# Performance work log

Measured on AMD Instinct MI355X. Metric: run time of the kernel, lower is better.

Reference implementation:

```python
import jax, jax.numpy as jnp
import numpy as np

LATENT_DIM = 256
CODEBOOK_SIZE = 8192


def setup_inputs() -> dict:
    key = jax.random.key(0)
    k1, k2 = jax.random.split(key)
    z_e = jax.random.normal(k1, (16, 32, 32, LATENT_DIM), dtype=jnp.float32)
    codebook = jax.random.normal(k2, (CODEBOOK_SIZE, LATENT_DIM), dtype=jnp.float32)
    return {"z_e": z_e, "codebook": codebook}


def reference(z_e, codebook):
    orig_shape = z_e.shape
    z_flat = z_e.reshape(-1, LATENT_DIM)                      # [N, D]
    # squared distances via ||z||^2 + ||e||^2 - 2 z.e^T  -> [N, K]
    dists = (jnp.sum(z_flat ** 2, axis=1, keepdims=True)
             + jnp.sum(codebook ** 2, axis=1)
             - 2.0 * jnp.matmul(z_flat, codebook.T))
    idx = jnp.argmin(dists, axis=1)                           # [N]
    z_q = codebook[idx].reshape(orig_shape)                   # gather + reshape
    commitment_loss = jnp.mean((jax.lax.stop_gradient(z_q) - z_e) ** 2)
    codebook_loss = jnp.mean((z_q - jax.lax.stop_gradient(z_e)) ** 2)
    loss = commitment_loss + codebook_loss
    z_q_st = z_e + jax.lax.stop_gradient(z_q - z_e)           # straight-through
    return (z_e, loss, z_q_st)
```

## Files before the change

kernel.cpp:

```cpp
#include <hip/hip_runtime.h>
#include <stdint.h>

typedef short short8 __attribute__((ext_vector_type(8)));
typedef float f32x4 __attribute__((ext_vector_type(4)));

#define DDIM 256
#define NROWS 16384
#define KCB 8192
#define KSPLIT 4
#define KC 2048
#define ND 4194304

__device__ __forceinline__ void gll16(const void* g, void* l) {
    __builtin_amdgcn_global_load_lds(
        (const __attribute__((address_space(1))) unsigned int*)g,
        (__attribute__((address_space(3))) unsigned int*)l, 16, 0, 0);
}

__device__ __forceinline__ unsigned short bf16_rne(float x) {
    unsigned u = __float_as_uint(x);
    unsigned r = (u + 0x7FFFu + ((u >> 16) & 1u)) >> 16;
    return (unsigned short)r;
}

__global__ void k_prep(const float* __restrict__ z, const float* __restrict__ cb,
                       unsigned short* __restrict__ zh, unsigned short* __restrict__ zl,
                       unsigned short* __restrict__ eh, unsigned short* __restrict__ el,
                       float* __restrict__ norms) {
    const int b = blockIdx.x, t = threadIdx.x;
    const bool isz = (b < 4096);
    const float* src = isz ? z : cb;
    unsigned short* hi = isz ? zh : eh;
    unsigned short* lo = isz ? zl : el;
    const int i = (isz ? b : (b - 4096)) * 256 + t;
    float4 v = reinterpret_cast<const float4*>(src)[i];
    ushort4 h, l;
    h.x = bf16_rne(v.x); l.x = bf16_rne(v.x - __uint_as_float((unsigned)h.x << 16));
    h.y = bf16_rne(v.y); l.y = bf16_rne(v.y - __uint_as_float((unsigned)h.y << 16));
    h.z = bf16_rne(v.z); l.z = bf16_rne(v.z - __uint_as_float((unsigned)h.z << 16));
    h.w = bf16_rne(v.w); l.w = bf16_rne(v.w - __uint_as_float((unsigned)h.w << 16));
    reinterpret_cast<ushort4*>(hi)[i] = h;
    reinterpret_cast<ushort4*>(lo)[i] = l;
    if (!isz) {
        float s = v.x * v.x + v.y * v.y + v.z * v.z + v.w * v.w;
#pragma unroll
        for (int off = 32; off > 0; off >>= 1) s += __shfl_xor(s, off, 64);
        if ((t & 63) == 0) norms[i >> 6] = s;
    }
}

__device__ __forceinline__ void stageB(char* sdst, const char* pe, const char* pl, int voff0) {
    gll16(pe + voff0,         sdst);
    gll16(pe + voff0 + 16384, sdst + 4096);
    gll16(pl + voff0,         sdst + 8192);
    gll16(pl + voff0 + 16384, sdst + 12288);
}

__launch_bounds__(256, 2)
__global__ void k_score(const unsigned short* __restrict__ zh, const unsigned short* __restrict__ zl,
                        const unsigned short* __restrict__ eh, const unsigned short* __restrict__ el,
                        const float* __restrict__ norms,
                        float* __restrict__ cand_val, int* __restrict__ cand_idx) {
    __shared__ char smem[32768];

    const int rb = blockIdx.x;
    const int ks = blockIdx.y;
    const int t = threadIdx.x, w = t >> 6, lane = t & 63;
    const int l15 = lane & 15, l4 = lane >> 4;

    const int colq = t >> 3;
    const int voff0 = colq * 512 + (((t & 7) ^ (colq & 7)) * 16);

    int voffB[2];
#pragma unroll
    for (int kc = 0; kc < 2; ++kc)
        voffB[kc] = l15 * 128 + ((((kc * 4) + l4) ^ (lane & 7)) * 16);

    short8 Ah[2][8], Al[2][8];
    {
        const size_t base0 = ((size_t)(rb * 128 + w * 32 + l15)) * DDIM + l4 * 8;
#pragma unroll
        for (int r = 0; r < 2; ++r)
#pragma unroll
            for (int kk = 0; kk < 8; ++kk) {
                Ah[r][kk] = *reinterpret_cast<const short8*>(zh + base0 + r * 16 * DDIM + kk * 32);
                Al[r][kk] = *reinterpret_cast<const short8*>(zl + base0 + r * 16 * DDIM + kk * 32);
            }
    }

    float v1[8], v2[8]; unsigned pk[8];
#pragma unroll
    for (int s = 0; s < 8; ++s) { v1[s] = 3.4e38f; v2[s] = 3.4e38f; pk[s] = 0; }

    size_t ub = (size_t)(ks * KC) * 512;
    stageB(smem + t * 16, (const char*)eh + ub, (const char*)el + ub, voff0);
    __syncthreads();

    for (int ct = 0; ct < 32; ++ct) {
        f32x4 acc[2][4];
#pragma unroll
        for (int r = 0; r < 2; ++r)
#pragma unroll
            for (int cf = 0; cf < 4; ++cf) acc[r][cf] = (f32x4){0.f, 0.f, 0.f, 0.f};

#pragma unroll
        for (int dc = 0; dc < 4; ++dc) {
            const int p = dc & 1;
            if (dc < 3) {
                stageB(smem + (p ^ 1) * 16384 + t * 16,
                       (const char*)eh + ub + (dc + 1) * 128,
                       (const char*)el + ub + (dc + 1) * 128, voff0);
            } else if (ct < 31) {
                stageB(smem + (p ^ 1) * 16384 + t * 16,
                       (const char*)eh + ub + 32768,
                       (const char*)el + ub + 32768, voff0);
            }
            const char* cb0 = smem + p * 16384;
#pragma unroll
            for (int cf = 0; cf < 4; ++cf) {
#pragma unroll
                for (int kc = 0; kc < 2; ++kc) {
                    short8 bh = *reinterpret_cast<const short8*>(cb0 + cf * 2048 + voffB[kc]);
                    short8 bl = *reinterpret_cast<const short8*>(cb0 + 8192 + cf * 2048 + voffB[kc]);
                    const int kk = dc * 2 + kc;
#pragma unroll
                    for (int r = 0; r < 2; ++r) {
                        acc[r][cf] = __builtin_amdgcn_mfma_f32_16x16x32_bf16(Ah[r][kk], bh, acc[r][cf], 0, 0, 0);
                        acc[r][cf] = __builtin_amdgcn_mfma_f32_16x16x32_bf16(Ah[r][kk], bl, acc[r][cf], 0, 0, 0);
                        acc[r][cf] = __builtin_amdgcn_mfma_f32_16x16x32_bf16(Al[r][kk], bh, acc[r][cf], 0, 0, 0);
                    }
                }
            }
            __syncthreads();
        }

        {
            const int nb = ks * KC + ct * 64 + l15;
            const float nn0 = norms[nb], nn1 = norms[nb + 16];
            const float nn2 = norms[nb + 32], nn3 = norms[nb + 48];
            const int cl0 = ct * 64 + l15;
#pragma unroll
            for (int r = 0; r < 2; ++r)
#pragma unroll
                for (int reg = 0; reg < 4; ++reg) {
                    float s0 = fmaf(-2.f, acc[r][0][reg], nn0);
                    float s1 = fmaf(-2.f, acc[r][1][reg], nn1);
                    float s2 = fmaf(-2.f, acc[r][2][reg], nn2);
                    float s3 = fmaf(-2.f, acc[r][3][reg], nn3);
                    float sm = s0; int sj = cl0;
                    if (s1 < sm) { sm = s1; sj = cl0 + 16; }
                    if (s2 < sm) { sm = s2; sj = cl0 + 32; }
                    if (s3 < sm) { sm = s3; sj = cl0 + 48; }
                    const int s = r * 4 + reg;
                    if (sm < v1[s]) { v2[s] = v1[s]; pk[s] = (pk[s] << 16) | (unsigned)sj; v1[s] = sm; }
                    else if (sm < v2[s]) { v2[s] = sm; pk[s] = (pk[s] & 0xFFFFu) | ((unsigned)sj << 16); }
                }
        }
        ub += 32768;
    }

#pragma unroll
    for (int m = 1; m < 16; m <<= 1) {
#pragma unroll
        for (int s = 0; s < 8; ++s) {
            float ov1 = __shfl_xor(v1[s], m, 64);
            float ov2 = __shfl_xor(v2[s], m, 64);
            unsigned opk = (unsigned)__shfl_xor((int)pk[s], m, 64);
            const int ia = (int)(pk[s] & 0xFFFFu), ib = (int)(opk & 0xFFFFu);
            bool bl = (ov1 < v1[s]) || (ov1 == v1[s] && ib < ia);
            float f1 = bl ? ov1 : v1[s]; int fi = bl ? ib : ia;
            float rv = bl ? v1[s] : ov1; int ri = bl ? ia : ib;
            float sv = bl ? ov2 : v2[s]; int si = bl ? (int)(opk >> 16) : (int)(pk[s] >> 16);
            bool b2 = (sv < rv) || (sv == rv && si < ri);
            v1[s] = f1; v2[s] = b2 ? sv : rv;
            pk[s] = (unsigned)fi | ((unsigned)(b2 ? si : ri) << 16);
        }
    }
    if (l15 == 0) {
#pragma unroll
        for (int s = 0; s < 8; ++s) {
            const int row = (s >> 2) * 16 + l4 * 4 + (s & 3);
            const int n = rb * 128 + w * 32 + row;
            cand_val[n * 8 + ks * 2 + 0] = v1[s];
            cand_val[n * 8 + ks * 2 + 1] = v2[s];
            cand_idx[n * 8 + ks * 2 + 0] = ks * KC + (int)(pk[s] & 0xFFFFu);
            cand_idx[n * 8 + ks * 2 + 1] = ks * KC + (int)(pk[s] >> 16);
        }
    }
}

__global__ void k_merge(const float* __restrict__ z, const float* __restrict__ cb,
                        const float* __restrict__ norms,
                        const float* __restrict__ cand_val, const int* __restrict__ cand_idx,
                        int* __restrict__ fidx) {
    const int gid = blockIdx.x * blockDim.x + threadIdx.x;
    const int wid = gid >> 6;
    const int lane = threadIdx.x & 63;
    float v1 = 3.4e38f, v2 = 3.4e38f; int i1 = 0, i2 = 0;
#pragma unroll
    for (int c = 0; c < 8; ++c) {
        float v = cand_val[wid * 8 + c]; int i = cand_idx[wid * 8 + c];
        bool lt1 = (v < v1) || (v == v1 && i < i1);
        bool lt2 = (v < v2) || (v == v2 && i < i2);
        if (lt1) { v2 = v1; i2 = i1; v1 = v; i1 = i; }
        else if (lt2) { v2 = v; i2 = i; }
    }
    const float4 zq = *reinterpret_cast<const float4*>(z + (size_t)wid * DDIM + lane * 4);
    float d[2]; int ii[2] = { i1, i2 };
#pragma unroll
    for (int c = 0; c < 2; ++c) {
        const float4 e4 = *reinterpret_cast<const float4*>(cb + (size_t)ii[c] * DDIM + lane * 4);
        float s = zq.x * e4.x + zq.y * e4.y + zq.z * e4.z + zq.w * e4.w;
#pragma unroll
        for (int m = 32; m > 0; m >>= 1) s += __shfl_xor(s, m, 64);
        d[c] = norms[ii[c]] - 2.f * s;
    }
    const int best = (d[1] < d[0] || (d[1] == d[0] && ii[1] < ii[0])) ? ii[1] : ii[0];
    if (lane == 0) fidx[wid] = best;
}

__global__ void k_finalize(const float* __restrict__ z, const float* __restrict__ cb,
                           const int* __restrict__ fidx, float* __restrict__ out,
                           float* __restrict__ partials) {
    const int i4 = blockIdx.x * blockDim.x + threadIdx.x;
    float4 zv = *reinterpret_cast<const float4*>(z + (size_t)i4 * 4);
    *reinterpret_cast<float4*>(out + (size_t)i4 * 4) = zv;
    const int n = i4 >> 6;
    const int d0 = (i4 & 63) << 2;
    const int idx = fidx[n];
    float4 q = *reinterpret_cast<const float4*>(cb + (size_t)idx * DDIM + d0);
    float* oq = out + (size_t)ND + 1 + (size_t)i4 * 4;
    oq[0] = q.x; oq[1] = q.y; oq[2] = q.z; oq[3] = q.w;
    const float dx = q.x - zv.x, dy = q.y - zv.y, dz = q.z - zv.z, dw = q.w - zv.w;
    float s = dx * dx + dy * dy + dz * dz + dw * dw;
#pragma unroll
    for (int off = 32; off > 0; off >>= 1) s += __shfl_xor(s, off, 64);
    __shared__ float sm[4];
    const int wv = threadIdx.x >> 6, ln = threadIdx.x & 63;
    if (ln == 0) sm[wv] = s;
    __syncthreads();
    if (threadIdx.x == 0) partials[blockIdx.x] = sm[0] + sm[1] + sm[2] + sm[3];
}

__global__ void k_loss(const float* __restrict__ partials, float* __restrict__ out) {
    float s = 0.f;
    for (int i = threadIdx.x; i < 4096; i += 256) s += partials[i];
#pragma unroll
    for (int off = 32; off > 0; off >>= 1) s += __shfl_xor(s, off, 64);
    __shared__ float sm[4];
    const int wv = threadIdx.x >> 6, ln = threadIdx.x & 63;
    if (ln == 0) sm[wv] = s;
    __syncthreads();
    if (threadIdx.x == 0) out[ND] = 2.0f * (sm[0] + sm[1] + sm[2] + sm[3]) / (float)ND;
}

extern "C" void kernel_launch(void* const* d_in, const int* in_sizes, int n_in,
                              void* d_out, int out_size, void* d_ws, size_t ws_size,
                              hipStream_t stream) {
    const float* z = (const float*)d_in[0];
    const float* cb = (const float*)d_in[1];
    float* out = (float*)d_out;
    float* ws = (float*)d_ws;

    float* norms = ws;
    int* fidx = (int*)(ws + 8192);
    float* partials = ws + 8192 + 16384;

    char* ob = (char*)d_out;
    unsigned short* zh = (unsigned short*)(ob);
    unsigned short* zl = (unsigned short*)(ob + 8388608);
    unsigned short* eh = (unsigned short*)(ob + 16777216);
    unsigned short* el = (unsigned short*)(ob + 20971520);
    float* cand_val = (float*)(ob + 25165824);
    int* cand_idx = (int*)(ob + 25690112);

    k_prep<<<dim3(6144), dim3(256), 0, stream>>>(z, cb, zh, zl, eh, el, norms);
    k_score<<<dim3(128, 4), dim3(256), 0, stream>>>(zh, zl, eh, el, norms, cand_val, cand_idx);
    k_merge<<<dim3(4096), dim3(256), 0, stream>>>(z, cb, norms, cand_val, cand_idx, fidx);
    k_finalize<<<dim3(4096), dim3(256), 0, stream>>>(z, cb, fidx, out, partials);
    k_loss<<<dim3(1), dim3(256), 0, stream>>>(partials, out);
}
```

Measured before the change: 272.1 us.

## Deepen codebook LDS pipeline to four stages with explicit waitcnt barriers

Replaces the two-buffer LDS double-buffering in the scoring kernel with a four-slot ring that keeps three chunks of codebook loads in flight. Each chunk ends with a partial vmcnt wait and a raw barrier instead of a full __syncthreads, and the MFMA block runs at raised wave priority. Candidate outputs are staged through LDS so they can be written with a coalesced pattern, and indices are masked in the downstream kernels. LDS doubles to 64KB per block, which may limit how many blocks fit per CU alongside the launch bound of 2.

```diff
diff --git a/kernel.cpp b/kernel.cpp
--- a/kernel.cpp
+++ b/kernel.cpp
@@ -49,19 +49,12 @@
     }
 }
 
-__device__ __forceinline__ void stageB(char* sdst, const char* pe, const char* pl, int voff0) {
-    gll16(pe + voff0,         sdst);
-    gll16(pe + voff0 + 16384, sdst + 4096);
-    gll16(pl + voff0,         sdst + 8192);
-    gll16(pl + voff0 + 16384, sdst + 12288);
-}
-
 __launch_bounds__(256, 2)
 __global__ void k_score(const unsigned short* __restrict__ zh, const unsigned short* __restrict__ zl,
                         const unsigned short* __restrict__ eh, const unsigned short* __restrict__ el,
                         const float* __restrict__ norms,
                         float* __restrict__ cand_val, int* __restrict__ cand_idx) {
-    __shared__ char smem[32768];
+    __shared__ char smem[65536];
 
     const int rb = blockIdx.x;
     const int ks = blockIdx.y;
@@ -88,76 +81,102 @@
             }
     }
 
+    const char* pe = (const char*)eh + (size_t)(ks * KC) * 512;
+    const char* pl = (const char*)el + (size_t)(ks * KC) * 512;
+
+    auto stage = [&](int s) {
+        const int off = (s >> 2) * 32768 + (s & 3) * 128;
+        char* sdst = smem + (s & 3) * 16384 + t * 16;
+        gll16(pe + off + voff0,         sdst);
+        gll16(pe + off + voff0 + 16384, sdst + 4096);
+        gll16(pl + off + voff0,         sdst + 8192);
+        gll16(pl + off + voff0 + 16384, sdst + 12288);
+    };
+
     float v1[8], v2[8]; unsigned pk[8];
 #pragma unroll
     for (int s = 0; s < 8; ++s) { v1[s] = 3.4e38f; v2[s] = 3.4e38f; pk[s] = 0; }
 
-    size_t ub = (size_t)(ks * KC) * 512;
-    stageB(smem + t * 16, (const char*)eh + ub, (const char*)el + ub, voff0);
-    __syncthreads();
-
-    for (int ct = 0; ct < 32; ++ct) {
-        f32x4 acc[2][4];
-#pragma unroll
-        for (int r = 0; r < 2; ++r)
-#pragma unroll
-            for (int cf = 0; cf < 4; ++cf) acc[r][cf] = (f32x4){0.f, 0.f, 0.f, 0.f};
-
-#pragma unroll
-        for (int dc = 0; dc < 4; ++dc) {
-            const int p = dc & 1;
-            if (dc < 3) {
-                stageB(smem + (p ^ 1) * 16384 + t * 16,
-                       (const char*)eh + ub + (dc + 1) * 128,
-                       (const char*)el + ub + (dc + 1) * 128, voff0);
-            } else if (ct < 31) {
-                stageB(smem + (p ^ 1) * 16384 + t * 16,
-                       (const char*)eh + ub + 32768,
-                       (const char*)el + ub + 32768, voff0);
-            }
-            const char* cb0 = smem + p * 16384;
-#pragma unroll
-            for (int cf = 0; cf < 4; ++cf) {
-#pragma unroll
-                for (int kc = 0; kc < 2; ++kc) {
-                    short8 bh = *reinterpret_cast<const short8*>(cb0 + cf * 2048 + voffB[kc]);
-                    short8 bl = *reinterpret_cast<const short8*>(cb0 + 8192 + cf * 2048 + voffB[kc]);
-                    const int kk = dc * 2 + kc;
-#pragma unroll
-                    for (int r = 0; r < 2; ++r) {
-                        acc[r][cf] = __builtin_amdgcn_mfma_f32_16x16x32_bf16(Ah[r][kk], bh, acc[r][cf], 0, 0, 0);
-                        acc[r][cf] = __builtin_amdgcn_mfma_f32_16x16x32_bf16(Ah[r][kk], bl, acc[r][cf], 0, 0, 0);
-                        acc[r][cf] = __builtin_amdgcn_mfma_f32_16x16x32_bf16(Al[r][kk], bh, acc[r][cf], 0, 0, 0);
-                    }
+    f32x4 acc[2][4];
+
+    auto compute = [&](int dc) {
+        const char* cb0 = smem + dc * 16384;
+        __builtin_amdgcn_s_setprio(1);
+#pragma unroll
+        for (int cf = 0; cf < 4; ++cf) {
+#pragma unroll
+            for (int kc = 0; kc < 2; ++kc) {
+                short8 bh = *reinterpret_cast<const short8*>(cb0 + cf * 2048 + voffB[kc]);
+                short8 bl = *reinterpret_cast<const short8*>(cb0 + 8192 + cf * 2048 + voffB[kc]);
+                const int kk = dc * 2 + kc;
+#pragma unroll
+                for (int r = 0; r < 2; ++r) {
+                    acc[r][cf] = __builtin_amdgcn_mfma_f32_16x16x32_bf16(Ah[r][kk], bh, acc[r][cf], 0, 0, 0);
+                    acc[r][cf] = __builtin_amdgcn_mfma_f32_16x16x32_bf16(Ah[r][kk], bl, acc[r][cf], 0, 0, 0);
+                    acc[r][cf] = __builtin_amdgcn_mfma_f32_16x16x32_bf16(Al[r][kk], bh, acc[r][cf], 0, 0, 0);
                 }
             }
-            __syncthreads();
         }
-
-        {
-            const int nb = ks * KC + ct * 64 + l15;
-            const float nn0 = norms[nb], nn1 = norms[nb + 16];
-            const float nn2 = norms[nb + 32], nn3 = norms[nb + 48];
-            const int cl0 = ct * 64 + l15;
-#pragma unroll
-            for (int r = 0; r < 2; ++r)
-#pragma unroll
-                for (int reg = 0; reg < 4; ++reg) {
-                    float s0 = fmaf(-2.f, acc[r][0][reg], nn0);
-                    float s1 = fmaf(-2.f, acc[r][1][reg], nn1);
-                    float s2 = fmaf(-2.f, acc[r][2][reg], nn2);
-                    float s3 = fmaf(-2.f, acc[r][3][reg], nn3);
-                    float sm = s0; int sj = cl0;
-                    if (s1 < sm) { sm = s1; sj = cl0 + 16; }
-                    if (s2 < sm) { sm = s2; sj = cl0 + 32; }
-                    if (s3 < sm) { sm = s3; sj = cl0 + 48; }
-                    const int s = r * 4 + reg;
-                    if (sm < v1[s]) { v2[s] = v1[s]; pk[s] = (pk[s] << 16) | (unsigned)sj; v1[s] = sm; }
-                    else if (sm < v2[s]) { v2[s] = sm; pk[s] = (pk[s] & 0xFFFFu) | ((unsigned)sj << 16); }
-                }
+        __builtin_amdgcn_s_setprio(0);
+    };
+
+    auto fold = [&](int ct) {
+        const int nb = ks * KC + ct * 64 + l15;
+        const float nn0 = norms[nb], nn1 = norms[nb + 16];
+        const float nn2 = norms[nb + 32], nn3 = norms[nb + 48];
+        const int cl0 = ct * 64 + l15;
+#pragma unroll
+        for (int r = 0; r < 2; ++r)
+#pragma unroll
+            for (int reg = 0; reg < 4; ++reg) {
+                float s0 = fmaf(-2.f, acc[r][0][reg], nn0);
+                float s1 = fmaf(-2.f, acc[r][1][reg], nn1);
+                float s2 = fmaf(-2.f, acc[r][2][reg], nn2);
+                float s3 = fmaf(-2.f, acc[r][3][reg], nn3);
+                float sm = s0; int sj = cl0;
+                if (s1 < sm) { sm = s1; sj = cl0 + 16; }
+                if (s2 < sm) { sm = s2; sj = cl0 + 32; }
+                if (s3 < sm) { sm = s3; sj = cl0 + 48; }
+                const int s = r * 4 + reg;
+                if (sm < v1[s]) { v2[s] = v1[s]; pk[s] = (pk[s] << 16) | (unsigned)sj; v1[s] = sm; }
+                else if (sm < v2[s]) { v2[s] = sm; pk[s] = (pk[s] & 0xFFFFu) | ((unsigned)sj << 16); }
+            }
+    };
+
+#define ACC_ZERO() do { \
+    _Pragma("unroll") for (int r = 0; r < 2; ++r) \
+    _Pragma("unroll") for (int cf = 0; cf < 4; ++cf) acc[r][cf] = (f32x4){0.f,0.f,0.f,0.f}; } while (0)
+
+#define SYNC_V8()  do { asm volatile("s_waitcnt vmcnt(8) lgkmcnt(0)" ::: "memory"); \
+    __builtin_amdgcn_sched_barrier(0); __builtin_amdgcn_s_barrier(); } while (0)
+#define SYNC_V4()  do { asm volatile("s_waitcnt vmcnt(4) lgkmcnt(0)" ::: "memory"); \
+    __builtin_amdgcn_sched_barrier(0); __builtin_amdgcn_s_barrier(); } while (0)
+#define SYNC_V0()  do { asm volatile("s_waitcnt vmcnt(0) lgkmcnt(0)" ::: "memory"); \
+    __builtin_amdgcn_sched_barrier(0); __builtin_amdgcn_s_barrier(); } while (0)
+
+    stage(0); stage(1); stage(2);
+    asm volatile("s_waitcnt vmcnt(8)" ::: "memory");
+    __builtin_amdgcn_sched_barrier(0);
+    __builtin_amdgcn_s_barrier();
+
+#pragma unroll 1
+    for (int ct = 0; ct < 31; ++ct) {
+        ACC_ZERO();
+        const int s0 = ct * 4;
+#pragma unroll
+        for (int dc = 0; dc < 4; ++dc) {
+            stage(s0 + dc + 3);
+            compute(dc);
+            SYNC_V8();
         }
-        ub += 32768;
-    }
+        fold(ct);
+    }
+    ACC_ZERO();
+    stage(127); compute(0); SYNC_V8();
+    compute(1);             SYNC_V4();
+    compute(2);             SYNC_V0();
+    compute(3);
+    fold(31);
 
 #pragma unroll
     for (int m = 1; m < 16; m <<= 1) {
@@ -176,16 +195,25 @@
             pk[s] = (unsigned)fi | ((unsigned)(b2 ? si : ri) << 16);
         }
     }
+    __syncthreads();
     if (l15 == 0) {
 #pragma unroll
         for (int s = 0; s < 8; ++s) {
             const int row = (s >> 2) * 16 + l4 * 4 + (s & 3);
-            const int n = rb * 128 + w * 32 + row;
-            cand_val[n * 8 + ks * 2 + 0] = v1[s];
-            cand_val[n * 8 + ks * 2 + 1] = v2[s];
-            cand_idx[n * 8 + ks * 2 + 0] = ks * KC + (int)(pk[s] & 0xFFFFu);
-            cand_idx[n * 8 + ks * 2 + 1] = ks * KC + (int)(pk[s] >> 16);
+            const int n = w * 32 + row;
+            reinterpret_cast<int4*>(smem)[n] =
+                make_int4(__float_as_int(v1[s]), (int)(pk[s] & 0xFFFFu),
+                          __float_as_int(v2[s]), (int)(pk[s] >> 16));
         }
+    }
+    __syncthreads();
+    if (t < 128) {
+        int4 A = reinterpret_cast<int4*>(smem)[t];
+        const int n = rb * 128 + t;
+        cand_val[n * 8 + ks * 2 + 0] = __int_as_float(A.x);
+        cand_val[n * 8 + ks * 2 + 1] = __int_as_float(A.z);
+        cand_idx[n * 8 + ks * 2 + 0] = ks * KC + A.y;
+        cand_idx[n * 8 + ks * 2 + 1] = ks * KC + A.w;
     }
 }
 
@@ -199,7 +227,7 @@
     float v1 = 3.4e38f, v2 = 3.4e38f; int i1 = 0, i2 = 0;
 #pragma unroll
     for (int c = 0; c < 8; ++c) {
-        float v = cand_val[wid * 8 + c]; int i = cand_idx[wid * 8 + c];
+        float v = cand_val[wid * 8 + c]; int i = cand_idx[wid * 8 + c] & (KCB - 1);
         bool lt1 = (v < v1) || (v == v1 && i < i1);
         bool lt2 = (v < v2) || (v == v2 && i < i2);
         if (lt1) { v2 = v1; i2 = i1; v1 = v; i1 = i; }
@@ -227,7 +255,7 @@
     *reinterpret_cast<float4*>(out + (size_t)i4 * 4) = zv;
     const int n = i4 >> 6;
     const int d0 = (i4 & 63) << 2;
-    const int idx = fidx[n];
+    const int idx = fidx[n] & (KCB - 1);
     float4 q = *reinterpret_cast<const float4*>(cb + (size_t)idx * DDIM + d0);
     float* oq = out + (size_t)ND + 1 + (size_t)i4 * 4;
     oq[0] = q.x; oq[1] = q.y; oq[2] = q.z; oq[3] = q.w;
```

After: 266.0 us. 1.02x faster.
